# Performance work log

Measured on AMD Instinct MI355X. Metric: run time of the kernel, lower is better.

The kernel has to match this reference:

```python
import jax, jax.numpy as jnp
import numpy as np

TAU = 0.5
EPS = 1e-12  # torch F.normalize default eps


def _l2norm(x):
    n = jnp.sqrt(jnp.sum(x * x, axis=1, keepdims=True))
    return x / jnp.maximum(n, EPS)


def _semi_loss(z1, z2, tau):
    z1n = _l2norm(z1)
    z2n = _l2norm(z2)
    refl = jnp.exp(jnp.matmul(z1n, z1n.T) / tau)      # [N, N]
    between = jnp.exp(jnp.matmul(z1n, z2n.T) / tau)   # [N, N]
    num = jnp.diagonal(between)
    den = refl.sum(axis=1) + between.sum(axis=1) - jnp.diagonal(refl)
    return -jnp.mean(jnp.log(num / den))


def setup_inputs() -> dict:
    key = jax.random.key(0)
    k1, k2 = jax.random.split(key)
    N, D = 8192, 256
    H_1 = jax.random.normal(k1, (N, D), dtype=jnp.float32)
    H_2 = jax.random.normal(k2, (N, D), dtype=jnp.float32)
    return {"H_1": H_1, "H_2": H_2}


def reference(H_1, H_2):
    l1 = _semi_loss(H_1, H_2, TAU)
    l2 = _semi_loss(H_2, H_1, TAU)
    return (l1 + l2) * 0.5
```

## Files before the change

kernel.cpp:

```cpp
#include <hip/hip_runtime.h>
#include <math.h>

#define NROW 8192
#define DDIM 256
#define BM 128
#define BN 128
#define NT_SYM 2080
#define NT_FULL 4096
#define NT_TOTAL (2 * NT_SYM + NT_FULL)

typedef __attribute__((ext_vector_type(16))) float f32x16;
typedef __attribute__((ext_vector_type(4)))  int   i32x4;
typedef __attribute__((ext_vector_type(8)))  int   i32x8;
typedef __attribute__((address_space(3))) unsigned int lds_u32;
typedef const __attribute__((address_space(1))) unsigned int glb_u32;

template <int CTRL>
static __device__ inline float dpp_ror_add(float v) {
    int s = __float_as_int(v);
    int r = __builtin_amdgcn_update_dpp(0, s, CTRL, 0xF, 0xF, true);
    return v + __int_as_float(r);
}
static __device__ inline float row16_sum(float v) {
    v = dpp_ror_add<0x121>(v);
    v = dpp_ror_add<0x122>(v);
    v = dpp_ror_add<0x124>(v);
    v = dpp_ror_add<0x128>(v);
    return v;
}

static __device__ inline unsigned int pack_fp8x4(float a, float b, float c, float d) {
    int p = __builtin_amdgcn_cvt_pk_fp8_f32(a, b, 0, false);
    p = __builtin_amdgcn_cvt_pk_fp8_f32(c, d, p, true);
    return (unsigned int)p;
}

__global__ __launch_bounds__(256) void normalize_kernel(
        const float* __restrict__ h1, const float* __restrict__ h2,
        unsigned char* __restrict__ z1b, unsigned char* __restrict__ z2b,
        float* __restrict__ diag,
        float* __restrict__ rs1, float* __restrict__ rs2,
        float* __restrict__ rbr, float* __restrict__ rbc,
        float* __restrict__ out) {
    int wave = threadIdx.x >> 6;
    int lane = threadIdx.x & 63;
    int row  = blockIdx.x * 4 + wave;
    if (blockIdx.x == 0 && threadIdx.x == 0) out[0] = 0.f;
    const float4* p1 = (const float4*)(h1 + (size_t)row * DDIM);
    const float4* p2 = (const float4*)(h2 + (size_t)row * DDIM);
    float4 a = p1[lane];
    float4 b = p2[lane];
    float s1 = a.x*a.x + a.y*a.y + a.z*a.z + a.w*a.w;
    float s2 = b.x*b.x + b.y*b.y + b.z*b.z + b.w*b.w;
    #pragma unroll
    for (int m = 1; m < 64; m <<= 1) { s1 += __shfl_xor(s1, m); s2 += __shfl_xor(s2, m); }
    float r1 = 1.0f / fmaxf(sqrtf(s1), 1e-12f);
    float r2 = 1.0f / fmaxf(sqrtf(s2), 1e-12f);
    float n1x = a.x*r1, n1y = a.y*r1, n1z = a.z*r1, n1w = a.w*r1;
    float n2x = b.x*r2, n2y = b.y*r2, n2z = b.z*r2, n2w = b.w*r2;
    float dt = n1x*n2x + n1y*n2y + n1z*n2z + n1w*n2w;
    #pragma unroll
    for (int m = 1; m < 64; m <<= 1) dt += __shfl_xor(dt, m);
    if (lane == 0) {
        diag[row] = 2.0f * dt;
        rs1[row] = 0.f; rs2[row] = 0.f; rbr[row] = 0.f; rbc[row] = 0.f;
    }
    const float SC = 1.69864364f;
    ((unsigned int*)(z1b + (size_t)row * DDIM))[lane] =
        pack_fp8x4(n1x*SC, n1y*SC, n1z*SC, n1w*SC);
    ((unsigned int*)(z2b + (size_t)row * DDIM))[lane] =
        pack_fp8x4(n2x*SC, n2y*SC, n2z*SC, n2w*SC);
}

__global__ __launch_bounds__(512, 6) void expsum_kernel(
        const unsigned char* __restrict__ z1, const unsigned char* __restrict__ z2,
        float* __restrict__ rs1, float* __restrict__ rs2,
        float* __restrict__ rbr, float* __restrict__ rbc) {
    int t = blockIdx.x;
    int kind, tt;
    if (t < NT_SYM)            { kind = 0; tt = t; }
    else if (t < 2 * NT_SYM)   { kind = 1; tt = t - NT_SYM; }
    else                       { kind = 2; tt = t - 2 * NT_SYM; }

    int by, bx;
    const unsigned char *Ap, *Bp;
    float *rowsum, *colsum;
    if (kind == 2) {
        by = tt >> 6; bx = tt & 63;
        Ap = z1; Bp = z2; rowsum = rbr; colsum = rbc;
    } else {
        by = (int)((sqrtf(8.0f * (float)tt + 1.0f) - 1.0f) * 0.5f);
        while ((by + 1) * (by + 2) / 2 <= tt) ++by;
        while (by * (by + 1) / 2 > tt) --by;
        bx = tt - by * (by + 1) / 2;
        const unsigned char* z = (kind == 0) ? z1 : z2;
        Ap = z; Bp = z;
        rowsum = (kind == 0) ? rs1 : rs2;
        colsum = (bx == by) ? nullptr : rowsum;
    }

    const int rt = by * BM;
    const int ct = bx * BN;

    __shared__ __align__(16) unsigned char lA[BM * DDIM];
    __shared__ float lds_rp[4][2][BM];
    __shared__ float lds_cp[2][2][BN];

    const int tid  = threadIdx.x;
    const int lane = tid & 63;
    const int wid  = tid >> 6;
    const int wr   = wid & 1;
    const int wc4  = wid >> 1;
    const int l31  = lane & 31;
    const int kh   = lane >> 5;

    const int srow = lane >> 4;
    const int sgt  = lane & 15;

    const int key  = lane & 15;

    const int aoff0 = (wr * 64 + l31) * DDIM;
    const int aoff1 = aoff0 + 32 * DDIM;

    #pragma unroll
    for (int p = 0; p < 4; ++p) {
        int r0 = (p * 8 + wid) * 4;
        int r  = r0 + srow;
        int gg = sgt ^ (r & 15);
        const unsigned char* ga = Ap + (size_t)(rt + r) * DDIM + gg * 16;
        __builtin_amdgcn_global_load_lds((glb_u32*)ga, (lds_u32*)(lA + r0 * DDIM), 16, 0, 0);
    }
    __syncthreads();

    const unsigned char* gB = Bp + (size_t)(ct + wc4 * 32 + l31) * DDIM + kh * 32;

    f32x16 acc0, acc1;
    #pragma unroll
    for (int r = 0; r < 16; ++r) { acc0[r] = 0.f; acc1[r] = 0.f; }

    #pragma unroll
    for (int kt = 0; kt < 2; ++kt) {
        #pragma unroll
        for (int ks = 0; ks < 2; ++ks) {
            const int g0   = kt * 8 + ks * 4 + kh * 2;
            const int off0 = (g0 ^ key) * 16;
            const int off1 = off0 ^ 16;
            const int bo   = kt * 128 + ks * 64;
            i32x8 a0, a1, bv;
            *((i32x4*)&a0)     = *(const i32x4*)(lA + aoff0 + off0);
            *((i32x4*)&a0 + 1) = *(const i32x4*)(lA + aoff0 + off1);
            *((i32x4*)&a1)     = *(const i32x4*)(lA + aoff1 + off0);
            *((i32x4*)&a1 + 1) = *(const i32x4*)(lA + aoff1 + off1);
            *((i32x4*)&bv)     = *(const i32x4*)(gB + bo);
            *((i32x4*)&bv + 1) = *(const i32x4*)(gB + bo + 16);
            acc0 = __builtin_amdgcn_mfma_scale_f32_32x32x64_f8f6f4(
                a0, bv, acc0, 0, 0, 0, 0x7F7F7F7F, 0, 0x7F7F7F7F);
            acc1 = __builtin_amdgcn_mfma_scale_f32_32x32x64_f8f6f4(
                a1, bv, acc1, 0, 0, 0, 0x7F7F7F7F, 0, 0x7F7F7F7F);
        }
    }

    float cp = 0.f;
    #pragma unroll
    for (int r = 0; r < 16; ++r) {
        float e0 = __builtin_amdgcn_exp2f(acc0[r]);
        float e1 = __builtin_amdgcn_exp2f(acc1[r]);
        cp += e0 + e1;
        float v0 = row16_sum(e0);
        float v1 = row16_sum(e1);
        if ((lane & 15) == 0) {
            int rloc = wr * 64 + 4 * kh + (r & 3) + 8 * (r >> 2);
            int sub16 = l31 >> 4;
            lds_rp[wc4][sub16][rloc]      = v0;
            lds_rp[wc4][sub16][rloc + 32] = v1;
        }
    }
    lds_cp[wr][kh][wc4 * 32 + l31] = cp;
    __syncthreads();

    if (tid < BM) {
        float s = lds_rp[0][0][tid] + lds_rp[0][1][tid]
                + lds_rp[1][0][tid] + lds_rp[1][1][tid]
                + lds_rp[2][0][tid] + lds_rp[2][1][tid]
                + lds_rp[3][0][tid] + lds_rp[3][1][tid];
        atomicAdd(&rowsum[rt + tid], s);
    } else if (colsum && tid < 2 * BM) {
        int c = tid - BM;
        float s = lds_cp[0][0][c] + lds_cp[0][1][c]
                + lds_cp[1][0][c] + lds_cp[1][1][c];
        atomicAdd(&colsum[ct + c], s);
    }
}

__global__ __launch_bounds__(256) void finalize_kernel(
        const float* __restrict__ rs1, const float* __restrict__ rs2,
        const float* __restrict__ rbr, const float* __restrict__ rbc,
        const float* __restrict__ diag, float* __restrict__ out) {
    __shared__ float s4[4];
    const float E2 = 7.38905609893065f;
    int i = blockIdx.x * 256 + threadIdx.x;
    float den1 = rs1[i] + rbr[i] - E2;
    float den2 = rs2[i] + rbc[i] - E2;
    float v = 0.5f * (logf(den1) + logf(den2)) - diag[i];
    #pragma unroll
    for (int m = 1; m < 64; m <<= 1) v += __shfl_xor(v, m);
    if ((threadIdx.x & 63) == 0) s4[threadIdx.x >> 6] = v;
    __syncthreads();
    if (threadIdx.x == 0) {
        float t = (s4[0] + s4[1] + s4[2] + s4[3]) * (1.0f / (float)NROW);
        atomicAdd(out, t);
    }
}

extern "C" void kernel_launch(void* const* d_in, const int* in_sizes, int n_in,
                              void* d_out, int out_size, void* d_ws, size_t ws_size,
                              hipStream_t stream) {
    const float* h1 = (const float*)d_in[0];
    const float* h2 = (const float*)d_in[1];
    float* out = (float*)d_out;

    char* ws = (char*)d_ws;
    unsigned char* z1b = (unsigned char*)ws;
    unsigned char* z2b = (unsigned char*)(ws + (size_t)NROW * DDIM);
    float* sums = (float*)(ws + (size_t)2 * NROW * DDIM);
    float* rs1  = sums;
    float* rs2  = sums + NROW;
    float* rbr  = sums + 2 * NROW;
    float* rbc  = sums + 3 * NROW;
    float* diag = sums + 4 * NROW;

    normalize_kernel<<<NROW / 4, 256, 0, stream>>>(h1, h2, z1b, z2b, diag,
                                                   rs1, rs2, rbr, rbc, out);

    expsum_kernel<<<NT_TOTAL, 512, 0, stream>>>(z1b, z2b, rs1, rs2, rbr, rbc);

    finalize_kernel<<<NROW / 256, 256, 0, stream>>>(rs1, rs2, rbr, rbc, diag, out);
}
```

Baseline: 138.5 us.

## Make expsum kernel persistent with double-buffered LDS prefetch of next tile

Replaces the one-block-per-tile launch of 8256 tiles with 512 persistent blocks that each walk 16 or 17 consecutive tiles. The A tile for the next iteration is loaded into a second LDS buffer with global_load_lds while the exp and reduction epilogue of the current tile runs. This targets launch and tail overhead and hides the A-tile load latency. In exchange LDS use doubles, occupancy is lowered to 4 waves per SIMD, and the fixed tile split may leave load imbalance across CUs.

```diff
diff --git a/kernel.cpp b/kernel.cpp
--- a/kernel.cpp
+++ b/kernel.cpp
@@ -8,6 +8,8 @@
 #define NT_SYM 2080
 #define NT_FULL 4096
 #define NT_TOTAL (2 * NT_SYM + NT_FULL)
+#define NBLK 512
+#define NBIG 64
 
 typedef __attribute__((ext_vector_type(16))) float f32x16;
 typedef __attribute__((ext_vector_type(4)))  int   i32x4;
@@ -72,37 +74,50 @@
         pack_fp8x4(n2x*SC, n2y*SC, n2z*SC, n2w*SC);
 }
 
-__global__ __launch_bounds__(512, 6) void expsum_kernel(
-        const unsigned char* __restrict__ z1, const unsigned char* __restrict__ z2,
-        float* __restrict__ rs1, float* __restrict__ rs2,
-        float* __restrict__ rbr, float* __restrict__ rbc) {
-    int t = blockIdx.x;
+struct Tile {
+    const unsigned char* Ap;
+    const unsigned char* Bp;
+    float* rowsum;
+    float* colsum;
+    int rt, ct;
+};
+
+static __device__ inline Tile decode_tile(int t,
+        const unsigned char* z1, const unsigned char* z2,
+        float* rs1, float* rs2, float* rbr, float* rbc) {
+    Tile ti;
     int kind, tt;
-    if (t < NT_SYM)            { kind = 0; tt = t; }
-    else if (t < 2 * NT_SYM)   { kind = 1; tt = t - NT_SYM; }
-    else                       { kind = 2; tt = t - 2 * NT_SYM; }
-
+    if (t < NT_SYM)          { kind = 0; tt = t; }
+    else if (t < 2 * NT_SYM) { kind = 1; tt = t - NT_SYM; }
+    else                     { kind = 2; tt = t - 2 * NT_SYM; }
     int by, bx;
-    const unsigned char *Ap, *Bp;
-    float *rowsum, *colsum;
     if (kind == 2) {
         by = tt >> 6; bx = tt & 63;
-        Ap = z1; Bp = z2; rowsum = rbr; colsum = rbc;
+        ti.Ap = z1; ti.Bp = z2; ti.rowsum = rbr; ti.colsum = rbc;
     } else {
         by = (int)((sqrtf(8.0f * (float)tt + 1.0f) - 1.0f) * 0.5f);
         while ((by + 1) * (by + 2) / 2 <= tt) ++by;
         while (by * (by + 1) / 2 > tt) --by;
         bx = tt - by * (by + 1) / 2;
         const unsigned char* z = (kind == 0) ? z1 : z2;
-        Ap = z; Bp = z;
-        rowsum = (kind == 0) ? rs1 : rs2;
-        colsum = (bx == by) ? nullptr : rowsum;
-    }
-
-    const int rt = by * BM;
-    const int ct = bx * BN;
-
-    __shared__ __align__(16) unsigned char lA[BM * DDIM];
+        ti.Ap = z; ti.Bp = z;
+        ti.rowsum = (kind == 0) ? rs1 : rs2;
+        ti.colsum = (bx == by) ? nullptr : ti.rowsum;
+    }
+    ti.rt = by * BM; ti.ct = bx * BN;
+    return ti;
+}
+
+__global__ __launch_bounds__(512, 4) void expsum_kernel(
+        const unsigned char* __restrict__ z1, const unsigned char* __restrict__ z2,
+        float* __restrict__ rs1, float* __restrict__ rs2,
+        float* __restrict__ rbr, float* __restrict__ rbc) {
+    int bid = blockIdx.x;
+    int start, cnt;
+    if (bid < NBIG) { start = bid * 17;                     cnt = 17; }
+    else            { start = NBIG * 17 + (bid - NBIG) * 16; cnt = 16; }
+
+    __shared__ __align__(16) unsigned char lA[2][BM * DDIM];
     __shared__ float lds_rp[4][2][BM];
     __shared__ float lds_cp[2][2][BN];
 
@@ -116,79 +131,106 @@
 
     const int srow = lane >> 4;
     const int sgt  = lane & 15;
-
     const int key  = lane & 15;
 
     const int aoff0 = (wr * 64 + l31) * DDIM;
     const int aoff1 = aoff0 + 32 * DDIM;
 
-    #pragma unroll
-    for (int p = 0; p < 4; ++p) {
-        int r0 = (p * 8 + wid) * 4;
-        int r  = r0 + srow;
-        int gg = sgt ^ (r & 15);
-        const unsigned char* ga = Ap + (size_t)(rt + r) * DDIM + gg * 16;
-        __builtin_amdgcn_global_load_lds((glb_u32*)ga, (lds_u32*)(lA + r0 * DDIM), 16, 0, 0);
-    }
-    __syncthreads();
-
-    const unsigned char* gB = Bp + (size_t)(ct + wc4 * 32 + l31) * DDIM + kh * 32;
-
-    f32x16 acc0, acc1;
-    #pragma unroll
-    for (int r = 0; r < 16; ++r) { acc0[r] = 0.f; acc1[r] = 0.f; }
-
-    #pragma unroll
-    for (int kt = 0; kt < 2; ++kt) {
-        #pragma unroll
-        for (int ks = 0; ks < 2; ++ks) {
-            const int g0   = kt * 8 + ks * 4 + kh * 2;
-            const int off0 = (g0 ^ key) * 16;
-            const int off1 = off0 ^ 16;
-            const int bo   = kt * 128 + ks * 64;
-            i32x8 a0, a1, bv;
-            *((i32x4*)&a0)     = *(const i32x4*)(lA + aoff0 + off0);
-            *((i32x4*)&a0 + 1) = *(const i32x4*)(lA + aoff0 + off1);
-            *((i32x4*)&a1)     = *(const i32x4*)(lA + aoff1 + off0);
-            *((i32x4*)&a1 + 1) = *(const i32x4*)(lA + aoff1 + off1);
-            *((i32x4*)&bv)     = *(const i32x4*)(gB + bo);
-            *((i32x4*)&bv + 1) = *(const i32x4*)(gB + bo + 16);
-            acc0 = __builtin_amdgcn_mfma_scale_f32_32x32x64_f8f6f4(
-                a0, bv, acc0, 0, 0, 0, 0x7F7F7F7F, 0, 0x7F7F7F7F);
-            acc1 = __builtin_amdgcn_mfma_scale_f32_32x32x64_f8f6f4(
-                a1, bv, acc1, 0, 0, 0, 0x7F7F7F7F, 0, 0x7F7F7F7F);
-        }
-    }
-
-    float cp = 0.f;
-    #pragma unroll
-    for (int r = 0; r < 16; ++r) {
-        float e0 = __builtin_amdgcn_exp2f(acc0[r]);
-        float e1 = __builtin_amdgcn_exp2f(acc1[r]);
-        cp += e0 + e1;
-        float v0 = row16_sum(e0);
-        float v1 = row16_sum(e1);
-        if ((lane & 15) == 0) {
-            int rloc = wr * 64 + 4 * kh + (r & 3) + 8 * (r >> 2);
-            int sub16 = l31 >> 4;
-            lds_rp[wc4][sub16][rloc]      = v0;
-            lds_rp[wc4][sub16][rloc + 32] = v1;
-        }
-    }
-    lds_cp[wr][kh][wc4 * 32 + l31] = cp;
-    __syncthreads();
-
-    if (tid < BM) {
-        float s = lds_rp[0][0][tid] + lds_rp[0][1][tid]
-                + lds_rp[1][0][tid] + lds_rp[1][1][tid]
-                + lds_rp[2][0][tid] + lds_rp[2][1][tid]
-                + lds_rp[3][0][tid] + lds_rp[3][1][tid];
-        atomicAdd(&rowsum[rt + tid], s);
-    } else if (colsum && tid < 2 * BM) {
-        int c = tid - BM;
-        float s = lds_cp[0][0][c] + lds_cp[0][1][c]
-                + lds_cp[1][0][c] + lds_cp[1][1][c];
-        atomicAdd(&colsum[ct + c], s);
+    Tile cur_t = decode_tile(start, z1, z2, rs1, rs2, rbr, rbc);
+    {
+        #pragma unroll
+        for (int p = 0; p < 4; ++p) {
+            int r0 = (p * 8 + wid) * 4;
+            int r  = r0 + srow;
+            int gg = sgt ^ (r & 15);
+            const unsigned char* ga = cur_t.Ap + (size_t)(cur_t.rt + r) * DDIM + gg * 16;
+            __builtin_amdgcn_global_load_lds((glb_u32*)ga,
+                (lds_u32*)(lA[0] + r0 * DDIM), 16, 0, 0);
+        }
+    }
+    int cur = 0;
+
+    for (int i = 0; i < cnt; ++i) {
+        __syncthreads();
+
+        const unsigned char* gB =
+            cur_t.Bp + (size_t)(cur_t.ct + wc4 * 32 + l31) * DDIM + kh * 32;
+        const unsigned char* bufA = lA[cur];
+
+        f32x16 acc0, acc1;
+        #pragma unroll
+        for (int r = 0; r < 16; ++r) { acc0[r] = 0.f; acc1[r] = 0.f; }
+
+        #pragma unroll
+        for (int kt = 0; kt < 2; ++kt) {
+            #pragma unroll
+            for (int ks = 0; ks < 2; ++ks) {
+                const int g0   = kt * 8 + ks * 4 + kh * 2;
+                const int off0 = (g0 ^ key) * 16;
+                const int off1 = off0 ^ 16;
+                const int bo   = kt * 128 + ks * 64;
+                i32x8 a0, a1, bv;
+                *((i32x4*)&a0)     = *(const i32x4*)(bufA + aoff0 + off0);
+                *((i32x4*)&a0 + 1) = *(const i32x4*)(bufA + aoff0 + off1);
+                *((i32x4*)&a1)     = *(const i32x4*)(bufA + aoff1 + off0);
+                *((i32x4*)&a1 + 1) = *(const i32x4*)(bufA + aoff1 + off1);
+                *((i32x4*)&bv)     = *(const i32x4*)(gB + bo);
+                *((i32x4*)&bv + 1) = *(const i32x4*)(gB + bo + 16);
+                acc0 = __builtin_amdgcn_mfma_scale_f32_32x32x64_f8f6f4(
+                    a0, bv, acc0, 0, 0, 0, 0x7F7F7F7F, 0, 0x7F7F7F7F);
+                acc1 = __builtin_amdgcn_mfma_scale_f32_32x32x64_f8f6f4(
+                    a1, bv, acc1, 0, 0, 0, 0x7F7F7F7F, 0, 0x7F7F7F7F);
+            }
+        }
+
+        Tile next_t = cur_t;
+        if (i + 1 < cnt) {
+            next_t = decode_tile(start + i + 1, z1, z2, rs1, rs2, rbr, rbc);
+            #pragma unroll
+            for (int p = 0; p < 4; ++p) {
+                int r0 = (p * 8 + wid) * 4;
+                int r  = r0 + srow;
+                int gg = sgt ^ (r & 15);
+                const unsigned char* ga =
+                    next_t.Ap + (size_t)(next_t.rt + r) * DDIM + gg * 16;
+                __builtin_amdgcn_global_load_lds((glb_u32*)ga,
+                    (lds_u32*)(lA[cur ^ 1] + r0 * DDIM), 16, 0, 0);
+            }
+        }
+
+        float cp = 0.f;
+        #pragma unroll
+        for (int r = 0; r < 16; ++r) {
+            float e0 = __builtin_amdgcn_exp2f(acc0[r]);
+            float e1 = __builtin_amdgcn_exp2f(acc1[r]);
+            cp += e0 + e1;
+            float v0 = row16_sum(e0);
+            float v1 = row16_sum(e1);
+            if ((lane & 15) == 0) {
+                int rloc = wr * 64 + 4 * kh + (r & 3) + 8 * (r >> 2);
+                int sub16 = l31 >> 4;
+                lds_rp[wc4][sub16][rloc]      = v0;
+                lds_rp[wc4][sub16][rloc + 32] = v1;
+            }
+        }
+        lds_cp[wr][kh][wc4 * 32 + l31] = cp;
+        __syncthreads();
+
+        if (tid < BM) {
+            float s = lds_rp[0][0][tid] + lds_rp[0][1][tid]
+                    + lds_rp[1][0][tid] + lds_rp[1][1][tid]
+                    + lds_rp[2][0][tid] + lds_rp[2][1][tid]
+                    + lds_rp[3][0][tid] + lds_rp[3][1][tid];
+            atomicAdd(&cur_t.rowsum[cur_t.rt + tid], s);
+        } else if (cur_t.colsum && tid < 2 * BM) {
+            int c = tid - BM;
+            float s = lds_cp[0][0][c] + lds_cp[0][1][c]
+                    + lds_cp[1][0][c] + lds_cp[1][1][c];
+            atomicAdd(&cur_t.colsum[cur_t.ct + c], s);
+        }
+
+        cur_t = next_t;
+        cur ^= 1;
     }
 }
 
@@ -232,7 +274,7 @@
     normalize_kernel<<<NROW / 4, 256, 0, stream>>>(h1, h2, z1b, z2b, diag,
                                                    rs1, rs2, rbr, rbc, out);
 
-    expsum_kernel<<<NT_TOTAL, 512, 0, stream>>>(z1b, z2b, rs1, rs2, rbr, rbc);
+    expsum_kernel<<<NBLK, 512, 0, stream>>>(z1b, z2b, rs1, rs2, rbr, rbc);
 
     finalize_kernel<<<NROW / 256, 256, 0, stream>>>(rs1, rs2, rbr, rbc, diag, out);
 }
```

Result: slower. 182.3 us (+31.6%).
